# Performance work log

Measured on AMD Instinct MI355X. Metric: run time of the kernel, lower is better.

The kernel has to match this reference:

```python
import jax, jax.numpy as jnp
import numpy as np

N_RAYS, N_SAMPLES = 4096, 64
N_HARM_XYZ, N_HARM_DIR = 10, 4
H_XYZ, H_DIR = 256, 128
N_LAYERS_XYZ = 8
SKIPS = (3,)
EMB_XYZ = N_HARM_XYZ * 2 * 3 + 3  # 63
EMB_DIR = N_HARM_DIR * 2 * 3 + 3  # 27


def harmonic(x, n_harmonics):
    freqs = 2.0 ** jnp.arange(n_harmonics, dtype=x.dtype)
    emb = (x[..., None] * freqs).reshape(*x.shape[:-1], -1)
    return jnp.concatenate([jnp.sin(emb), jnp.cos(emb), x], axis=-1)


def _linear_params(key, out_dim, in_dim):
    kw, kb = jax.random.split(key)
    s = 1.0 / np.sqrt(in_dim)
    W = jax.random.uniform(kw, (out_dim, in_dim), jnp.float32, -s, s)
    b = jax.random.uniform(kb, (out_dim,), jnp.float32, -s, s)
    return W, b


def setup_inputs() -> dict:
    key = jax.random.key(0)
    keys = jax.random.split(key, 16)
    inp = {
        'sample_points': jax.random.normal(keys[0], (N_RAYS, N_SAMPLES, 3), jnp.float32),
        'directions': jax.random.normal(keys[1], (N_RAYS, 3), jnp.float32),
    }
    # xyz MLP: layer 0: EMB_XYZ->H; layer i (i>=1): input H, or H+EMB_XYZ if (i-1) in SKIPS
    for i in range(N_LAYERS_XYZ):
        if i == 0:
            in_dim = EMB_XYZ
        elif (i - 1) in SKIPS:
            in_dim = H_XYZ + EMB_XYZ
        else:
            in_dim = H_XYZ
        W, b = _linear_params(keys[2 + i], H_XYZ, in_dim)
        inp[f'Wx{i}'], inp[f'bx{i}'] = W, b
    inp['Wd0'], inp['bd0'] = _linear_params(keys[10], H_DIR, H_XYZ + EMB_DIR)
    inp['Wden'], inp['bden'] = _linear_params(keys[11], 1, H_XYZ)
    inp['Wfeat'], inp['bfeat'] = _linear_params(keys[12], H_XYZ, H_XYZ)
    inp['Wrgb'], inp['brgb'] = _linear_params(keys[13], 3, H_DIR)
    return inp


def reference(sample_points, directions,
              Wx0, bx0, Wx1, bx1, Wx2, bx2, Wx3, bx3,
              Wx4, bx4, Wx5, bx5, Wx6, bx6, Wx7, bx7,
              Wd0, bd0, Wden, bden, Wfeat, bfeat, Wrgb, brgb):
    emb_x = harmonic(sample_points, N_HARM_XYZ)  # [N, S, 63]
    layers = [(Wx0, bx0), (Wx1, bx1), (Wx2, bx2), (Wx3, bx3),
              (Wx4, bx4), (Wx5, bx5), (Wx6, bx6), (Wx7, bx7)]
    x = emb_x
    for i, (W, b) in enumerate(layers):
        x = jax.nn.relu(jnp.einsum('nsi,oi->nso', x, W) + b)
        if i in SKIPS:
            x = jnp.concatenate([x, emb_x], axis=-1)
    density = jax.nn.relu(jnp.einsum('nsi,oi->nso', x, Wden) + bden)  # [N, S, 1]
    x = jax.nn.relu(jnp.einsum('nsi,oi->nso', x, Wfeat) + bfeat)
    dirs = jnp.broadcast_to(directions[:, None, :], (directions.shape[0], x.shape[1], 3))
    emb_d = harmonic(dirs, N_HARM_DIR)  # [N, S, 27]
    x = jnp.concatenate([x, emb_d], axis=-1)
    x = jax.nn.relu(jnp.einsum('nsi,oi->nso', x, Wd0) + bd0)
    rgb = jax.nn.sigmoid(jnp.einsum('nsi,oi->nso', x, Wrgb) + brgb)  # [N, S, 3]
    return jnp.concatenate([density, rgb], axis=-1)  # [N, S, 4]
```

## Files before the change

### kernel.cpp

```cpp
#include <hip/hip_runtime.h>
#include <hip/hip_bf16.h>
#include <math.h>

#define N_RAYS 4096
#define N_SAMPLES 64
#define M_TOTAL (N_RAYS * N_SAMPLES)
#define MTILE 128
#define NBLK (M_TOTAL / MTILE)
#define THREADS 512

#define OFF_W0 0
#define OFF_W1 16384
#define OFF_W2 81920
#define OFF_W3 147456
#define OFF_W4 212992
#define OFF_W5 294912
#define OFF_W6 360448
#define OFF_W7 425984
#define OFF_WF 491520
#define OFF_WD 557056

typedef __attribute__((ext_vector_type(8))) short bf16x8;
typedef __attribute__((ext_vector_type(4))) float f32x4;
typedef __attribute__((ext_vector_type(4))) unsigned short u16x4;

__device__ __forceinline__ unsigned short f2bf(float f) {
  __hip_bfloat16 h = __float2bfloat16(f);
  return *(unsigned short*)&h;
}
__device__ __forceinline__ float bf2f(unsigned short h) {
  union { unsigned u; float f; } v; v.u = ((unsigned)h) << 16;
  return v.f;
}

template<int STRIDE, int SWL>
__device__ __forceinline__ int sidx(int r, int c) {
  const int cc = (c < SWL) ? (c ^ ((r & 7) << 3)) : c;
  return r * STRIDE + cc;
}

template<int KPAD, int NF, int SI, int SWLI, int SO, int SWLO>
__device__ __forceinline__ void layer_mfma(
    const unsigned short* __restrict__ inb, int col0,
    unsigned short* __restrict__ outb,
    const unsigned short* __restrict__ W,
    const float* __restrict__ bias,
    int wave, int ln15, int lhi)
{
  f32x4 acc[8][NF];
#pragma unroll
  for (int m = 0; m < 8; ++m)
#pragma unroll
    for (int n = 0; n < NF; ++n)
      acc[m][n] = (f32x4){0.f, 0.f, 0.f, 0.f};

  const unsigned short* wr[NF];
#pragma unroll
  for (int n = 0; n < NF; ++n)
    wr[n] = W + (wave * (NF * 16) + n * 16 + ln15) * KPAD + lhi * 8;

  const int kb = col0 + lhi * 8;
#pragma unroll
  for (int k0 = 0; k0 < KPAD; k0 += 32) {
    bf16x8 w[NF];
#pragma unroll
    for (int n = 0; n < NF; ++n)
      w[n] = *(const bf16x8*)(wr[n] + k0);
#pragma unroll
    for (int g = 0; g < 2; ++g) {
      bf16x8 a[4];
#pragma unroll
      for (int mm = 0; mm < 4; ++mm)
        a[mm] = *(const bf16x8*)(inb + sidx<SI, SWLI>((g * 4 + mm) * 16 + ln15, kb + k0));
#pragma unroll
      for (int n = 0; n < NF; ++n)
#pragma unroll
        for (int mm = 0; mm < 4; ++mm)
          acc[g * 4 + mm][n] =
              __builtin_amdgcn_mfma_f32_16x16x32_bf16(w[n], a[mm], acc[g * 4 + mm][n], 0, 0, 0);
    }
  }

#pragma unroll
  for (int n = 0; n < NF; ++n) {
    const int feat0 = wave * (NF * 16) + n * 16 + lhi * 4;
    const f32x4 bb = *(const f32x4*)(bias + feat0);
#pragma unroll
    for (int m = 0; m < 8; ++m) {
      u16x4 pk;
#pragma unroll
      for (int r = 0; r < 4; ++r)
        pk[r] = f2bf(fmaxf(acc[m][n][r] + bb[r], 0.f));
      *(u16x4*)(outb + sidx<SO, SWLO>(m * 16 + ln15, feat0)) = pk;
    }
  }
}

struct NerfArgs {
  const float *sp, *dirs;
  const unsigned short* wp;
  const float *bx0, *bx1, *bx2, *bx3, *bx4, *bx5, *bx6, *bx7;
  const float *bd0, *Wden, *bden, *bfeat, *Wrgb, *brgb;
  float* out;
};

__global__ void __attribute__((amdgpu_flat_work_group_size(THREADS, THREADS),
                               amdgpu_waves_per_eu(2, 2)))
nerf_main(NerfArgs A) {
  extern __shared__ unsigned short lds[];
  unsigned short* buf0 = lds;
  unsigned short* buf1 = lds + 128 * 320;
  const int tid = threadIdx.x;
  const int wave = tid >> 6, lane = tid & 63;
  const int ln15 = lane & 15, lhi = lane >> 4;
  const int blk = blockIdx.x;

  {
    const int r = tid & 127, g = tid >> 7;
    if (g < 3) {
      const float x = A.sp[(blk * MTILE + r) * 3 + g];
      buf0[sidx<320, 320>(r, 256 + 60 + g)] = f2bf(x);
#pragma unroll
      for (int f = 0; f < 10; ++f) {
        const float ar = x * (float)(1 << f);
        buf0[sidx<320, 320>(r, 256 + g * 10 + f)]      = f2bf(sinf(ar));
        buf0[sidx<320, 320>(r, 256 + 30 + g * 10 + f)] = f2bf(cosf(ar));
      }
    } else {
      buf0[sidx<320, 320>(r, 319)] = 0;
    }
  }
  __syncthreads();

  const unsigned short* wp = A.wp;
  layer_mfma<64, 2, 320, 320, 288, 256>(buf0, 256, buf1, wp + OFF_W0, A.bx0, wave, ln15, lhi);
  __syncthreads();
  layer_mfma<256, 2, 288, 256, 320, 320>(buf1, 0, buf0, wp + OFF_W1, A.bx1, wave, ln15, lhi);
  __syncthreads();
  layer_mfma<256, 2, 320, 320, 288, 256>(buf0, 0, buf1, wp + OFF_W2, A.bx2, wave, ln15, lhi);
  __syncthreads();
  layer_mfma<256, 2, 288, 256, 320, 320>(buf1, 0, buf0, wp + OFF_W3, A.bx3, wave, ln15, lhi);
  __syncthreads();
  layer_mfma<320, 2, 320, 320, 288, 256>(buf0, 0, buf1, wp + OFF_W4, A.bx4, wave, ln15, lhi);
  __syncthreads();
  layer_mfma<256, 2, 288, 256, 320, 320>(buf1, 0, buf0, wp + OFF_W5, A.bx5, wave, ln15, lhi);
  __syncthreads();
  layer_mfma<256, 2, 320, 320, 288, 256>(buf0, 0, buf1, wp + OFF_W6, A.bx6, wave, ln15, lhi);
  __syncthreads();
  layer_mfma<256, 2, 288, 256, 320, 320>(buf1, 0, buf0, wp + OFF_W7, A.bx7, wave, ln15, lhi);
  __syncthreads();
  layer_mfma<256, 2, 320, 320, 288, 256>(buf0, 0, buf1, wp + OFF_WF, A.bfeat, wave, ln15, lhi);

  float dens = 0.f;
  {
    const int r = wave * 16 + ln15;
    float s = 0.f;
#pragma unroll
    for (int jj = 0; jj < 8; ++jj) {
      const bf16x8 ch = *(const bf16x8*)(buf0 + sidx<320, 320>(r, lhi * 64 + jj * 8));
#pragma unroll
      for (int e = 0; e < 8; ++e)
        s += bf2f((unsigned short)ch[e]) * A.Wden[lhi * 64 + jj * 8 + e];
    }
    s += __shfl_xor(s, 16);
    s += __shfl_xor(s, 32);
    dens = fmaxf(s + A.bden[0], 0.f);
  }
  if (tid < 64) {
    const int j = tid & 31, h = tid >> 5;
    const float* dp = A.dirs + (blk * 2 + h) * 3;
    float val = 0.f;
    if (j < 12)      { int d = j >> 2, f = j & 3;               val = sinf(dp[d] * (float)(1 << f)); }
    else if (j < 24) { int d = (j - 12) >> 2, f = (j - 12) & 3; val = cosf(dp[d] * (float)(1 << f)); }
    else if (j < 27) { val = dp[j - 24]; }
    buf0[sidx<320, 320>(h, 288 + j)] = f2bf(val);
  }
  __syncthreads();
  for (int idx = tid; idx < 128 * 32; idx += THREADS) {
    const int rr = idx >> 5, cc = idx & 31;
    buf1[sidx<288, 256>(rr, 256 + cc)] = buf0[sidx<320, 320>(rr >> 6, 288 + cc)];
  }
  __syncthreads();
  layer_mfma<288, 1, 288, 256, 320, 320>(buf1, 0, buf0, wp + OFF_WD, A.bd0, wave, ln15, lhi);
  __syncthreads();
  {
    const int r = wave * 16 + ln15;
    float s0 = 0.f, s1 = 0.f, s2 = 0.f;
#pragma unroll
    for (int jj = 0; jj < 4; ++jj) {
      const bf16x8 ch = *(const bf16x8*)(buf0 + sidx<320, 320>(r, lhi * 32 + jj * 8));
#pragma unroll
      for (int e = 0; e < 8; ++e) {
        const int k = lhi * 32 + jj * 8 + e;
        const float xv = bf2f((unsigned short)ch[e]);
        s0 += xv * A.Wrgb[k];
        s1 += xv * A.Wrgb[128 + k];
        s2 += xv * A.Wrgb[256 + k];
      }
    }
    s0 += __shfl_xor(s0, 16); s0 += __shfl_xor(s0, 32);
    s1 += __shfl_xor(s1, 16); s1 += __shfl_xor(s1, 32);
    s2 += __shfl_xor(s2, 16); s2 += __shfl_xor(s2, 32);
    if (lhi == 0) {
      f32x4 o;
      o[0] = dens;
      o[1] = 1.f / (1.f + expf(-(s0 + A.brgb[0])));
      o[2] = 1.f / (1.f + expf(-(s1 + A.brgb[1])));
      o[3] = 1.f / (1.f + expf(-(s2 + A.brgb[2])));
      *(f32x4*)(A.out + (blk * MTILE + r) * 4) = o;
    }
  }
}

struct PackDesc { const float* src; int out_dim, in_dim, kpad, dst_off; };
struct PackArgs { PackDesc d[10]; };

__global__ void __launch_bounds__(256) pack_weights(PackArgs P, unsigned short* dst) {
  const PackDesc pd = P.d[blockIdx.y];
  const int idx = blockIdx.x * 256 + threadIdx.x;
  const int tot = pd.out_dim * pd.kpad;
  if (idx >= tot) return;
  const int o = idx / pd.kpad;
  const int k = idx - o * pd.kpad;
  const float v = (k < pd.in_dim) ? pd.src[o * pd.in_dim + k] : 0.f;
  dst[pd.dst_off + idx] = f2bf(v);
}

extern "C" void kernel_launch(void* const* d_in, const int* in_sizes, int n_in,
                              void* d_out, int out_size, void* d_ws, size_t ws_size,
                              hipStream_t stream) {
  unsigned short* wpack = (unsigned short*)d_ws;

  const float* Wx[8]; const float* bx[8];
  for (int i = 0; i < 8; ++i) {
    Wx[i] = (const float*)d_in[2 + 2 * i];
    bx[i] = (const float*)d_in[3 + 2 * i];
  }

  PackArgs P;
  P.d[0] = { Wx[0], 256, 63, 64, OFF_W0 };
  P.d[1] = { Wx[1], 256, 256, 256, OFF_W1 };
  P.d[2] = { Wx[2], 256, 256, 256, OFF_W2 };
  P.d[3] = { Wx[3], 256, 256, 256, OFF_W3 };
  P.d[4] = { Wx[4], 256, 319, 320, OFF_W4 };
  P.d[5] = { Wx[5], 256, 256, 256, OFF_W5 };
  P.d[6] = { Wx[6], 256, 256, 256, OFF_W6 };
  P.d[7] = { Wx[7], 256, 256, 256, OFF_W7 };
  P.d[8] = { (const float*)d_in[22], 256, 256, 256, OFF_WF };
  P.d[9] = { (const float*)d_in[18], 128, 283, 288, OFF_WD };
  hipLaunchKernelGGL(pack_weights, dim3(320, 10), dim3(256), 0, stream, P, wpack);

  NerfArgs A;
  A.sp = (const float*)d_in[0];
  A.dirs = (const float*)d_in[1];
  A.wp = wpack;
  A.bx0 = bx[0]; A.bx1 = bx[1]; A.bx2 = bx[2]; A.bx3 = bx[3];
  A.bx4 = bx[4]; A.bx5 = bx[5]; A.bx6 = bx[6]; A.bx7 = bx[7];
  A.bd0 = (const float*)d_in[19];
  A.Wden = (const float*)d_in[20];
  A.bden = (const float*)d_in[21];
  A.bfeat = (const float*)d_in[23];
  A.Wrgb = (const float*)d_in[24];
  A.brgb = (const float*)d_in[25];
  A.out = (float*)d_out;

  const int lds_bytes = (128 * 320 + 128 * 288) * 2;
  hipFuncSetAttribute((const void*)nerf_main, hipFuncAttributeMaxDynamicSharedMemorySize, lds_bytes);
  hipLaunchKernelGGL(nerf_main, dim3(NBLK), dim3(THREADS), lds_bytes, stream, A);
}
```

Baseline: 481.8 us.

## Move harmonic embeddings into a separate LDS buffer with split-K MFMA layers

Hidden activations now live in two unpadded 256-wide ping-pong buffers, and the xyz and direction embeddings sit in their own swizzled 64-wide buffer. Layers that consume an embedding run a second K loop over that buffer instead of reading padded 288/320-wide rows. The direction-embedding step computes sin/cos directly into the embedding buffer, which removes one barrier and a copy pass. This cuts LDS footprint and gives every row a uniform swizzle, but skip layers now need weight rows whose packed layout matches the new split K order.

```diff
diff --git a/kernel.cpp b/kernel.cpp
--- a/kernel.cpp
+++ b/kernel.cpp
@@ -33,15 +33,15 @@
   return v.f;
 }
 
-template<int STRIDE, int SWL>
+template<int STRIDE>
 __device__ __forceinline__ int sidx(int r, int c) {
-  const int cc = (c < SWL) ? (c ^ ((r & 7) << 3)) : c;
-  return r * STRIDE + cc;
-}
-
-template<int KPAD, int NF, int SI, int SWLI, int SO, int SWLO>
+  return r * STRIDE + (c ^ ((r & 7) << 3));
+}
+
+template<int KPAD, int K2, int NF>
 __device__ __forceinline__ void layer_mfma(
-    const unsigned short* __restrict__ inb, int col0,
+    const unsigned short* __restrict__ inb,
+    const unsigned short* __restrict__ emb,
     unsigned short* __restrict__ outb,
     const unsigned short* __restrict__ W,
     const float* __restrict__ bias,
@@ -57,9 +57,9 @@
   const unsigned short* wr[NF];
 #pragma unroll
   for (int n = 0; n < NF; ++n)
-    wr[n] = W + (wave * (NF * 16) + n * 16 + ln15) * KPAD + lhi * 8;
-
-  const int kb = col0 + lhi * 8;
+    wr[n] = W + (wave * (NF * 16) + n * 16 + ln15) * (KPAD + K2) + lhi * 8;
+
+  const int kb = lhi * 8;
 #pragma unroll
   for (int k0 = 0; k0 < KPAD; k0 += 32) {
     bf16x8 w[NF];
@@ -71,7 +71,7 @@
       bf16x8 a[4];
 #pragma unroll
       for (int mm = 0; mm < 4; ++mm)
-        a[mm] = *(const bf16x8*)(inb + sidx<SI, SWLI>((g * 4 + mm) * 16 + ln15, kb + k0));
+        a[mm] = *(const bf16x8*)(inb + sidx<256>((g * 4 + mm) * 16 + ln15, kb + k0));
 #pragma unroll
       for (int n = 0; n < NF; ++n)
 #pragma unroll
@@ -80,6 +80,28 @@
               __builtin_amdgcn_mfma_f32_16x16x32_bf16(w[n], a[mm], acc[g * 4 + mm][n], 0, 0, 0);
     }
   }
+  if (K2 > 0) {
+#pragma unroll
+    for (int k0 = 0; k0 < K2; k0 += 32) {
+      bf16x8 w[NF];
+#pragma unroll
+      for (int n = 0; n < NF; ++n)
+        w[n] = *(const bf16x8*)(wr[n] + KPAD + k0);
+#pragma unroll
+      for (int g = 0; g < 2; ++g) {
+        bf16x8 a[4];
+#pragma unroll
+        for (int mm = 0; mm < 4; ++mm)
+          a[mm] = *(const bf16x8*)(emb + sidx<64>((g * 4 + mm) * 16 + ln15, kb + k0));
+#pragma unroll
+        for (int n = 0; n < NF; ++n)
+#pragma unroll
+          for (int mm = 0; mm < 4; ++mm)
+            acc[g * 4 + mm][n] =
+                __builtin_amdgcn_mfma_f32_16x16x32_bf16(w[n], a[mm], acc[g * 4 + mm][n], 0, 0, 0);
+      }
+    }
+  }
 
 #pragma unroll
   for (int n = 0; n < NF; ++n) {
@@ -91,7 +113,7 @@
 #pragma unroll
       for (int r = 0; r < 4; ++r)
         pk[r] = f2bf(fmaxf(acc[m][n][r] + bb[r], 0.f));
-      *(u16x4*)(outb + sidx<SO, SWLO>(m * 16 + ln15, feat0)) = pk;
+      *(u16x4*)(outb + sidx<256>(m * 16 + ln15, feat0)) = pk;
     }
   }
 }
@@ -109,7 +131,8 @@
 nerf_main(NerfArgs A) {
   extern __shared__ unsigned short lds[];
   unsigned short* buf0 = lds;
-  unsigned short* buf1 = lds + 128 * 320;
+  unsigned short* buf1 = lds + 128 * 256;
+  unsigned short* embr = lds + 2 * 128 * 256;
   const int tid = threadIdx.x;
   const int wave = tid >> 6, lane = tid & 63;
   const int ln15 = lane & 15, lhi = lane >> 4;
@@ -119,37 +142,38 @@
     const int r = tid & 127, g = tid >> 7;
     if (g < 3) {
       const float x = A.sp[(blk * MTILE + r) * 3 + g];
-      buf0[sidx<320, 320>(r, 256 + 60 + g)] = f2bf(x);
+      embr[sidx<64>(r, 60 + g)] = f2bf(x);
 #pragma unroll
       for (int f = 0; f < 10; ++f) {
         const float ar = x * (float)(1 << f);
-        buf0[sidx<320, 320>(r, 256 + g * 10 + f)]      = f2bf(sinf(ar));
-        buf0[sidx<320, 320>(r, 256 + 30 + g * 10 + f)] = f2bf(cosf(ar));
+        embr[sidx<64>(r, g * 10 + f)]      = f2bf(sinf(ar));
+        embr[sidx<64>(r, 30 + g * 10 + f)] = f2bf(cosf(ar));
       }
     } else {
-      buf0[sidx<320, 320>(r, 319)] = 0;
+      embr[sidx<64>(r, 63)] = 0;
     }
   }
   __syncthreads();
 
   const unsigned short* wp = A.wp;
-  layer_mfma<64, 2, 320, 320, 288, 256>(buf0, 256, buf1, wp + OFF_W0, A.bx0, wave, ln15, lhi);
-  __syncthreads();
-  layer_mfma<256, 2, 288, 256, 320, 320>(buf1, 0, buf0, wp + OFF_W1, A.bx1, wave, ln15, lhi);
-  __syncthreads();
-  layer_mfma<256, 2, 320, 320, 288, 256>(buf0, 0, buf1, wp + OFF_W2, A.bx2, wave, ln15, lhi);
-  __syncthreads();
-  layer_mfma<256, 2, 288, 256, 320, 320>(buf1, 0, buf0, wp + OFF_W3, A.bx3, wave, ln15, lhi);
-  __syncthreads();
-  layer_mfma<320, 2, 320, 320, 288, 256>(buf0, 0, buf1, wp + OFF_W4, A.bx4, wave, ln15, lhi);
-  __syncthreads();
-  layer_mfma<256, 2, 288, 256, 320, 320>(buf1, 0, buf0, wp + OFF_W5, A.bx5, wave, ln15, lhi);
-  __syncthreads();
-  layer_mfma<256, 2, 320, 320, 288, 256>(buf0, 0, buf1, wp + OFF_W6, A.bx6, wave, ln15, lhi);
-  __syncthreads();
-  layer_mfma<256, 2, 288, 256, 320, 320>(buf1, 0, buf0, wp + OFF_W7, A.bx7, wave, ln15, lhi);
-  __syncthreads();
-  layer_mfma<256, 2, 320, 320, 288, 256>(buf0, 0, buf1, wp + OFF_WF, A.bfeat, wave, ln15, lhi);
+  layer_mfma<0, 64, 2>(buf0, embr, buf1, wp + OFF_W0, A.bx0, wave, ln15, lhi);
+  __syncthreads();
+  layer_mfma<256, 0, 2>(buf1, nullptr, buf0, wp + OFF_W1, A.bx1, wave, ln15, lhi);
+  __syncthreads();
+  layer_mfma<256, 0, 2>(buf0, nullptr, buf1, wp + OFF_W2, A.bx2, wave, ln15, lhi);
+  __syncthreads();
+  layer_mfma<256, 0, 2>(buf1, nullptr, buf0, wp + OFF_W3, A.bx3, wave, ln15, lhi);
+  __syncthreads();
+  layer_mfma<256, 64, 2>(buf0, embr, buf1, wp + OFF_W4, A.bx4, wave, ln15, lhi);
+  __syncthreads();
+  layer_mfma<256, 0, 2>(buf1, nullptr, buf0, wp + OFF_W5, A.bx5, wave, ln15, lhi);
+  __syncthreads();
+  layer_mfma<256, 0, 2>(buf0, nullptr, buf1, wp + OFF_W6, A.bx6, wave, ln15, lhi);
+  __syncthreads();
+  layer_mfma<256, 0, 2>(buf1, nullptr, buf0, wp + OFF_W7, A.bx7, wave, ln15, lhi);
+  __syncthreads();
+
+  layer_mfma<256, 0, 2>(buf0, nullptr, buf1, wp + OFF_WF, A.bfeat, wave, ln15, lhi);
 
   float dens = 0.f;
   {
@@ -157,7 +181,7 @@
     float s = 0.f;
 #pragma unroll
     for (int jj = 0; jj < 8; ++jj) {
-      const bf16x8 ch = *(const bf16x8*)(buf0 + sidx<320, 320>(r, lhi * 64 + jj * 8));
+      const bf16x8 ch = *(const bf16x8*)(buf0 + sidx<256>(r, lhi * 64 + jj * 8));
 #pragma unroll
       for (int e = 0; e < 8; ++e)
         s += bf2f((unsigned short)ch[e]) * A.Wden[lhi * 64 + jj * 8 + e];
@@ -166,29 +190,32 @@
     s += __shfl_xor(s, 32);
     dens = fmaxf(s + A.bden[0], 0.f);
   }
-  if (tid < 64) {
-    const int j = tid & 31, h = tid >> 5;
-    const float* dp = A.dirs + (blk * 2 + h) * 3;
-    float val = 0.f;
-    if (j < 12)      { int d = j >> 2, f = j & 3;               val = sinf(dp[d] * (float)(1 << f)); }
-    else if (j < 24) { int d = (j - 12) >> 2, f = (j - 12) & 3; val = cosf(dp[d] * (float)(1 << f)); }
-    else if (j < 27) { val = dp[j - 24]; }
-    buf0[sidx<320, 320>(h, 288 + j)] = f2bf(val);
-  }
-  __syncthreads();
-  for (int idx = tid; idx < 128 * 32; idx += THREADS) {
-    const int rr = idx >> 5, cc = idx & 31;
-    buf1[sidx<288, 256>(rr, 256 + cc)] = buf0[sidx<320, 320>(rr >> 6, 288 + cc)];
-  }
-  __syncthreads();
-  layer_mfma<288, 1, 288, 256, 320, 320>(buf1, 0, buf0, wp + OFF_WD, A.bd0, wave, ln15, lhi);
+  {
+    const float* dp = A.dirs + blk * 2 * 3;
+    const float dx[2] = {dp[0], dp[3]}, dy[2] = {dp[1], dp[4]}, dz[2] = {dp[2], dp[5]};
+    for (int idx = tid; idx < 128 * 32; idx += THREADS) {
+      const int rr = idx >> 5, cc = idx & 31, h = rr >> 6;
+      float val = 0.f;
+      if (cc < 24) {
+        const int j = (cc < 12) ? cc : cc - 12;
+        const int d = j >> 2, f = j & 3;
+        const float cv = (d == 0 ? dx[h] : (d == 1 ? dy[h] : dz[h])) * (float)(1 << f);
+        val = (cc < 12) ? sinf(cv) : cosf(cv);
+      } else if (cc < 27) {
+        val = (cc == 24) ? dx[h] : (cc == 25 ? dy[h] : dz[h]);
+      }
+      embr[sidx<64>(rr, cc)] = f2bf(val);
+    }
+  }
+  __syncthreads();
+  layer_mfma<256, 32, 1>(buf1, embr, buf0, wp + OFF_WD, A.bd0, wave, ln15, lhi);
   __syncthreads();
   {
     const int r = wave * 16 + ln15;
     float s0 = 0.f, s1 = 0.f, s2 = 0.f;
 #pragma unroll
     for (int jj = 0; jj < 4; ++jj) {
-      const bf16x8 ch = *(const bf16x8*)(buf0 + sidx<320, 320>(r, lhi * 32 + jj * 8));
+      const bf16x8 ch = *(const bf16x8*)(buf0 + sidx<256>(r, lhi * 32 + jj * 8));
 #pragma unroll
       for (int e = 0; e < 8; ++e) {
         const int k = lhi * 32 + jj * 8 + e;
@@ -264,7 +291,7 @@
   A.brgb = (const float*)d_in[25];
   A.out = (float*)d_out;
 
-  const int lds_bytes = (128 * 320 + 128 * 288) * 2;
+  const int lds_bytes = (2 * 128 * 256 + 128 * 64) * 2;
   hipFuncSetAttribute((const void*)nerf_main, hipFuncAttributeMaxDynamicSharedMemorySize, lds_bytes);
   hipLaunchKernelGGL(nerf_main, dim3(NBLK), dim3(THREADS), lds_bytes, stream, A);
 }
```

Result: slower. 503.3 us (+4.4%).
